# Kernel tuning notes

Measured on AMD Instinct MI355X. Metric: run time of the kernel, lower is better.

The kernel has to match this reference:

```python
import jax, jax.numpy as jnp
import numpy as np

D_MODEL = 768
MIMO_RANK = 4


def setup_inputs() -> dict:
    key = jax.random.key(0)
    ks = jax.random.split(key, 6)
    B, T, D, R = 2, 2048, D_MODEL, MIMO_RANK
    x = jax.random.normal(ks[0], (B, T, D), dtype=jnp.float32)
    norm_w = jnp.ones((D,), dtype=jnp.float32)
    W_in = jax.random.normal(ks[1], (D * R * 2, D), dtype=jnp.float32) * 0.02
    W_out = jax.random.normal(ks[2], (D, D), dtype=jnp.float32) * 0.02
    a_param = jax.random.normal(ks[3], (D, R, 2), dtype=jnp.float32) * 0.12
    b_param = jax.random.normal(ks[4], (D, R, 2), dtype=jnp.float32) * 0.15
    c_param = jax.random.normal(ks[5], (D, R, 2), dtype=jnp.float32) * 0.15
    return {"x": x, "norm_w": norm_w, "W_in": W_in, "W_out": W_out,
            "a_param": a_param, "b_param": b_param, "c_param": c_param}


def reference(x, norm_w, W_in, W_out, a_param, b_param, c_param):
    B, T, D = x.shape
    R = a_param.shape[1]
    # RMSNorm
    xn = x * jax.lax.rsqrt(jnp.mean(x * x, axis=-1, keepdims=True) + 1e-6) * norm_w
    # in_proj -> interleaved complex MIMO input u: [B,T,D,R,2]
    u = (xn @ W_in.T).reshape(B, T, D, R, 2)
    # coefficients (tanh-bounded; |a| scaled by 0.97 for stability)
    a = jnp.tanh(a_param) * 0.97
    b = jnp.tanh(b_param)
    c = jnp.tanh(c_param)
    ac = jax.lax.complex(a[..., 0], a[..., 1])  # [D,R]
    bc = jax.lax.complex(b[..., 0], b[..., 1])
    cc = jax.lax.complex(c[..., 0], c[..., 1])
    uc = jax.lax.complex(u[..., 0], u[..., 1])  # [B,T,D,R]
    # linear complex recurrence s_t = a * s_{t-1} + b * u_t, zero init state,
    # parallelized with an associative scan over time.
    bu = bc[None, None] * uc
    A = jnp.broadcast_to(ac[None, None], bu.shape)

    def comb(l, r):
        return (l[0] * r[0], r[0] * l[1] + r[1])

    _, s = jax.lax.associative_scan(comb, (A, bu), axis=1)  # [B,T,D,R] complex
    # output mix: real part of c * h, summed over MIMO rank -> [B,T,D]
    y = jnp.real(cc[None, None] * s).sum(axis=-1)
    return y @ W_out.T
```

## Files before the change

kernel.cpp:

```cpp
#include <hip/hip_runtime.h>
#include <hip/hip_bf16.h>
#include <stdint.h>

#define BATCH 2
#define TT 2048
#define DM 768
#define RR 4
#define M_TOK 4096
#define NFEAT 6144
#define NCH 6144
#define CHUNK 64
#define NCHUNK 32

typedef __attribute__((ext_vector_type(8))) short short8;
typedef __attribute__((ext_vector_type(4))) float float4v;

__device__ inline float bf2f(uint32_t bits16) {
    union { uint32_t u; float f; } x; x.u = bits16 << 16; return x.f;
}

typedef const __attribute__((address_space(1))) void* gptr_t;
typedef __attribute__((address_space(3))) void* lptr_t;

__device__ inline void async_ld16(const void* g, void* l) {
    __builtin_amdgcn_global_load_lds((gptr_t)(uintptr_t)g, (lptr_t)(uintptr_t)l,
                                     16, 0, 0);
}

__device__ inline void store_c(__hip_bfloat16* C, size_t idx, float v) {
    C[idx] = __float2bfloat16(v);
}
__device__ inline void store_c(float* C, size_t idx, float v) { C[idx] = v; }

__device__ inline uint2 pack4bf(float a, float b, float c, float d) {
    union { __hip_bfloat16 h[4]; uint2 u; } o;
    o.h[0] = __float2bfloat16(a); o.h[1] = __float2bfloat16(b);
    o.h[2] = __float2bfloat16(c); o.h[3] = __float2bfloat16(d);
    return o.u;
}

__device__ inline float2 cmul(float2 a, float2 b) {
    return make_float2(a.x * b.x - a.y * b.y, a.x * b.y + a.y * b.x);
}
__device__ inline float2 cmad(float2 a, float2 b, float2 c) {
    return make_float2(a.x * b.x - a.y * b.y + c.x,
                       a.x * b.y + a.y * b.x + c.y);
}
__device__ inline float2 csq(float2 a) {
    return make_float2(a.x * a.x - a.y * a.y, 2.f * a.x * a.y);
}

__device__ inline void cstep(float& sr, float& si, float2 a, float2 bb,
                             uint32_t uw) {
    float ur = bf2f(uw & 0xffffu), ui = bf2f(uw >> 16);
    float tr = bb.x * ur - bb.y * ui;
    float ti = bb.x * ui + bb.y * ur;
    float nr = a.x * sr - a.y * si + tr;
    float ni = a.x * si + a.y * sr + ti;
    sr = nr; si = ni;
}

__global__ __launch_bounds__(256) void prep_rms(
    const float* __restrict__ x, const float* __restrict__ w,
    const float* __restrict__ W_in, const float* __restrict__ W_out,
    const float* __restrict__ ap, const float* __restrict__ bp,
    const float* __restrict__ cp,
    __hip_bfloat16* __restrict__ xn,
    __hip_bfloat16* __restrict__ Win_bf, __hip_bfloat16* __restrict__ Wout_bf,
    float2* __restrict__ ac, float2* __restrict__ bc,
    float2* __restrict__ cc, float2* __restrict__ aQ,
    float2* __restrict__ aL) {
    int bid = blockIdx.x;
    int tid = threadIdx.x;
    if (bid < M_TOK) {
        __shared__ float wsum[3];
        float4 v = make_float4(0.f, 0.f, 0.f, 0.f);
        if (tid < 192) v = ((const float4*)(x + (size_t)bid * DM))[tid];
        float ss = v.x * v.x + v.y * v.y + v.z * v.z + v.w * v.w;
        #pragma unroll
        for (int o = 1; o < 64; o <<= 1) ss += __shfl_xor(ss, o);
        if (tid < 192 && (tid & 63) == 0) wsum[tid >> 6] = ss;
        __syncthreads();
        if (tid < 192) {
            float tot = wsum[0] + wsum[1] + wsum[2];
            float scale = rsqrtf(tot * (1.f / DM) + 1e-6f);
            float4 wv = ((const float4*)w)[tid];
            ((uint2*)(xn + (size_t)bid * DM))[tid] =
                pack4bf(v.x * scale * wv.x, v.y * scale * wv.y,
                        v.z * scale * wv.z, v.w * scale * wv.w);
        }
        return;
    }
    const int N1 = NFEAT * DM / 4;
    const int N2 = DM * DM / 4;
    int i = (bid - M_TOK) * 256 + tid;
    if (i < N1) {
        float4 v = ((const float4*)W_in)[i];
        ((uint2*)Win_bf)[i] = pack4bf(v.x, v.y, v.z, v.w);
    } else if (i < N1 + N2) {
        int k = i - N1;
        float4 v = ((const float4*)W_out)[k];
        ((uint2*)Wout_bf)[k] = pack4bf(v.x, v.y, v.z, v.w);
    }
    if (i < DM * RR) {
        float ar = tanhf(ap[2 * i])     * 0.97f;
        float ai = tanhf(ap[2 * i + 1]) * 0.97f;
        ac[i] = make_float2(ar, ai);
        bc[i] = make_float2(tanhf(bp[2 * i]), tanhf(bp[2 * i + 1]));
        cc[i] = make_float2(tanhf(cp[2 * i]), tanhf(cp[2 * i + 1]));
        float xr = ar, xi = ai;
        #pragma unroll
        for (int k = 0; k < 4; ++k) {
            float nr = xr * xr - xi * xi;
            float ni = 2.f * xr * xi;
            xr = nr; xi = ni;
        }
        aQ[i] = make_float2(xr, xi);
        #pragma unroll
        for (int k = 0; k < 2; ++k) {
            float nr = xr * xr - xi * xi;
            float ni = 2.f * xr * xi;
            xr = nr; xi = ni;
        }
        aL[i] = make_float2(xr, xi);
    }
}

template <int BM, int BN, int BK, typename OutT>
__device__ inline void gemm_body(
    const __hip_bfloat16* __restrict__ A, const __hip_bfloat16* __restrict__ B,
    OutT* __restrict__ C, int K, int ldc) {
    constexpr int MI = BM / 32;
    constexpr int NJ = BN / 32;
    constexpr int CPR = BK / 8;
    __shared__ __attribute__((aligned(16))) __hip_bfloat16 lA[BM * BK];
    __shared__ __attribute__((aligned(16))) __hip_bfloat16 lB[BN * BK];
    const int tid  = threadIdx.x;
    const int lane = tid & 63;
    const int wave = tid >> 6;
    const int quad = lane >> 4;
    const int l15  = lane & 15;
    const int wm = (wave >> 1) * (BM / 2);
    const int wn = (wave & 1) * (BN / 2);
    const int m0 = blockIdx.y * BM;
    const int n0 = blockIdx.x * BN;

    float4v acc[MI][NJ] = {};

    for (int k0 = 0; k0 < K; k0 += BK) {
        __syncthreads();
        #pragma unroll
        for (int it = 0; it < BM * CPR / 256; ++it) {
            int p = it * 256 + tid;
            int row = p / CPR;
            int cg = (p & (CPR - 1)) ^ (row & (CPR - 1));
            async_ld16(A + (size_t)(m0 + row) * K + k0 + cg * 8, lA + p * 8);
        }
        #pragma unroll
        for (int it = 0; it < BN * CPR / 256; ++it) {
            int p = it * 256 + tid;
            int row = p / CPR;
            int cg = (p & (CPR - 1)) ^ (row & (CPR - 1));
            async_ld16(B + (size_t)(n0 + row) * K + k0 + cg * 8, lB + p * 8);
        }
        __syncthreads();
        #pragma unroll
        for (int s = 0; s < BK / 32; ++s) {
            short8 af[MI], bfr[NJ];
            #pragma unroll
            for (int i = 0; i < MI; ++i) {
                int r = wm + i * 16 + l15;
                int c = (s * 4 + quad) ^ (r & (CPR - 1));
                af[i] = *(const short8*)(lA + r * BK + c * 8);
            }
            #pragma unroll
            for (int j = 0; j < NJ; ++j) {
                int r = wn + j * 16 + l15;
                int c = (s * 4 + quad) ^ (r & (CPR - 1));
                bfr[j] = *(const short8*)(lB + r * BK + c * 8);
            }
            #pragma unroll
            for (int i = 0; i < MI; ++i)
                #pragma unroll
                for (int j = 0; j < NJ; ++j)
                    acc[i][j] = __builtin_amdgcn_mfma_f32_16x16x32_bf16(
                        af[i], bfr[j], acc[i][j], 0, 0, 0);
        }
    }
    #pragma unroll
    for (int i = 0; i < MI; ++i)
        #pragma unroll
        for (int j = 0; j < NJ; ++j)
            #pragma unroll
            for (int rg = 0; rg < 4; ++rg) {
                int row = m0 + wm + i * 16 + quad * 4 + rg;
                int col = n0 + wn + j * 16 + l15;
                store_c(C, (size_t)row * ldc + col, acc[i][j][rg]);
            }
}

__global__ __launch_bounds__(256) void gemm_in(
    const __hip_bfloat16* __restrict__ A, const __hip_bfloat16* __restrict__ B,
    __hip_bfloat16* __restrict__ C, int K) {
    gemm_body<128, 128, 64, __hip_bfloat16>(A, B, C, K, NFEAT);
}

__global__ __launch_bounds__(256) void gemm_out(
    const __hip_bfloat16* __restrict__ A, const __hip_bfloat16* __restrict__ B,
    float* __restrict__ C, int K) {
    gemm_body<64, 64, 128, float>(A, B, C, K, DM);
}

__global__ __launch_bounds__(256) void scan_local2(
    const uint4* __restrict__ u4,
    const float2* __restrict__ ac, const float2* __restrict__ bc,
    const float2* __restrict__ cc,
    __hip_bfloat16* __restrict__ y_local,
    float2* __restrict__ chunkEnd) {
    __shared__ float2 se[1024];
    const int tid   = threadIdx.x;
    const int d_loc = tid & 31;
    const int s8    = tid >> 5;
    const int bd    = blockIdx.x;
    const int b     = bd >= 24;
    const int dg    = bd - b * 24;
    const int d_g   = dg * 32 + d_loc;
    const int cb    = d_g * RR;
    const int j     = blockIdx.y;

    float2 a0 = ac[cb], a1 = ac[cb + 1], a2 = ac[cb + 2], a3 = ac[cb + 3];
    float2 b0 = bc[cb], b1 = bc[cb + 1], b2 = bc[cb + 2], b3 = bc[cb + 3];
    float2 c0 = cc[cb], c1 = cc[cb + 1], c2 = cc[cb + 2], c3 = cc[cb + 3];

    const int token0 = b * TT + j * CHUNK + s8 * 8;
    const size_t base = (size_t)token0 * DM + d_g;

    uint4 uw[8];
    #pragma unroll
    for (int i = 0; i < 8; ++i) uw[i] = u4[base + (size_t)i * DM];
    float s0r = 0, s0i = 0, s1r = 0, s1i = 0;
    float s2r = 0, s2i = 0, s3r = 0, s3i = 0;
    float yloc[8];
    #pragma unroll
    for (int i = 0; i < 8; ++i) {
        cstep(s0r, s0i, a0, b0, uw[i].x);
        cstep(s1r, s1i, a1, b1, uw[i].y);
        cstep(s2r, s2i, a2, b2, uw[i].z);
        cstep(s3r, s3i, a3, b3, uw[i].w);
        yloc[i] = c0.x * s0r - c0.y * s0i + c1.x * s1r - c1.y * s1i
                + c2.x * s2r - c2.y * s2i + c3.x * s3r - c3.y * s3i;
    }
    se[tid * 4]     = make_float2(s0r, s0i);
    se[tid * 4 + 1] = make_float2(s1r, s1i);
    se[tid * 4 + 2] = make_float2(s2r, s2i);
    se[tid * 4 + 3] = make_float2(s3r, s3i);
    __syncthreads();

    float2 aE0 = csq(csq(csq(a0))), aE1 = csq(csq(csq(a1)));
    float2 aE2 = csq(csq(csq(a2))), aE3 = csq(csq(csq(a3)));
    float2 C0 = make_float2(0, 0), C1 = C0, C2 = C0, C3 = C0;
    for (int k = 0; k < s8; ++k) {
        int kb = (k * 32 + d_loc) * 4;
        C0 = cmad(C0, aE0, se[kb]);
        C1 = cmad(C1, aE1, se[kb + 1]);
        C2 = cmad(C2, aE2, se[kb + 2]);
        C3 = cmad(C3, aE3, se[kb + 3]);
    }
    if (s8 == 7) {
        size_t eb = (size_t)j * NCH + b * (DM * RR) + cb;
        chunkEnd[eb]     = cmad(C0, aE0, make_float2(s0r, s0i));
        chunkEnd[eb + 1] = cmad(C1, aE1, make_float2(s1r, s1i));
        chunkEnd[eb + 2] = cmad(C2, aE2, make_float2(s2r, s2i));
        chunkEnd[eb + 3] = cmad(C3, aE3, make_float2(s3r, s3i));
    }
    float2 q0 = cmul(cmul(c0, C0), a0);
    float2 q1 = cmul(cmul(c1, C1), a1);
    float2 q2 = cmul(cmul(c2, C2), a2);
    float2 q3 = cmul(cmul(c3, C3), a3);
    #pragma unroll
    for (int i = 0; i < 8; ++i) {
        float yv = yloc[i] + q0.x + q1.x + q2.x + q3.x;
        y_local[base + (size_t)i * DM] = __float2bfloat16(yv);
        q0 = cmul(q0, a0); q1 = cmul(q1, a1);
        q2 = cmul(q2, a2); q3 = cmul(q3, a3);
    }
}

__global__ __launch_bounds__(256) void scan_fix(
    const __hip_bfloat16* __restrict__ y_local,
    const float2* __restrict__ ac, const float2* __restrict__ cc,
    const float2* __restrict__ aQp, const float2* __restrict__ aLp,
    const float2* __restrict__ chunkEnd,
    __hip_bfloat16* __restrict__ y) {
    int g = blockIdx.x * 256 + threadIdx.x;
    int j = blockIdx.y;
    int z = blockIdx.z;
    int b = g >= DM;
    int d = g - b * DM;
    int cb = d * RR;
    float2 a0 = ac[cb], a1 = ac[cb + 1], a2 = ac[cb + 2], a3 = ac[cb + 3];
    float2 aL0 = aLp[cb], aL1 = aLp[cb + 1], aL2 = aLp[cb + 2], aL3 = aLp[cb + 3];
    float2 k0 = make_float2(0, 0), k1 = k0, k2 = k0, k3 = k0;
    for (int jj = 0; jj < j; ++jj) {
        size_t eb = (size_t)jj * NCH + b * (DM * RR) + cb;
        float2 e0 = chunkEnd[eb],     e1 = chunkEnd[eb + 1];
        float2 e2 = chunkEnd[eb + 2], e3 = chunkEnd[eb + 3];
        k0 = cmad(k0, aL0, e0); k1 = cmad(k1, aL1, e1);
        k2 = cmad(k2, aL2, e2); k3 = cmad(k3, aL3, e3);
    }
    float2 q0 = cmul(cmul(cc[cb],     k0), a0);
    float2 q1 = cmul(cmul(cc[cb + 1], k1), a1);
    float2 q2 = cmul(cmul(cc[cb + 2], k2), a2);
    float2 q3 = cmul(cmul(cc[cb + 3], k3), a3);
    float2 aQ0 = aQp[cb], aQ1 = aQp[cb + 1], aQ2 = aQp[cb + 2], aQ3 = aQp[cb + 3];
    for (int zz = 0; zz < z; ++zz) {
        q0 = cmul(q0, aQ0); q1 = cmul(q1, aQ1);
        q2 = cmul(q2, aQ2); q3 = cmul(q3, aQ3);
    }
    size_t base = ((size_t)(b * TT + j * CHUNK + z * 16)) * DM + d;
    #pragma unroll 4
    for (int i = 0; i < 16; ++i) {
        float yv = bf2f(((const uint16_t*)y_local)[base + (size_t)i * DM])
                 + q0.x + q1.x + q2.x + q3.x;
        y[base + (size_t)i * DM] = __float2bfloat16(yv);
        q0 = cmul(q0, a0); q1 = cmul(q1, a1);
        q2 = cmul(q2, a2); q3 = cmul(q3, a3);
    }
}

extern "C" void kernel_launch(void* const* d_in, const int* in_sizes, int n_in,
                              void* d_out, int out_size, void* d_ws,
                              size_t ws_size, hipStream_t stream) {
    const float* x      = (const float*)d_in[0];
    const float* norm_w = (const float*)d_in[1];
    const float* W_in   = (const float*)d_in[2];
    const float* W_out  = (const float*)d_in[3];
    const float* a_p    = (const float*)d_in[4];
    const float* b_p    = (const float*)d_in[5];
    const float* c_p    = (const float*)d_in[6];
    float* out = (float*)d_out;

    char* ws = (char*)d_ws;
    size_t off = 0;
    auto alloc = [&](size_t bytes) {
        void* p = ws + off;
        off += (bytes + 255) & ~(size_t)255;
        return p;
    };
    __hip_bfloat16* Win_bf  = (__hip_bfloat16*)alloc((size_t)NFEAT * DM * 2);
    __hip_bfloat16* Wout_bf = (__hip_bfloat16*)alloc((size_t)DM * DM * 2);
    __hip_bfloat16* xn      = (__hip_bfloat16*)alloc((size_t)M_TOK * DM * 2);
    __hip_bfloat16* u       = (__hip_bfloat16*)alloc((size_t)M_TOK * NFEAT * 2);
    __hip_bfloat16* y_local = (__hip_bfloat16*)alloc((size_t)M_TOK * DM * 2);
    __hip_bfloat16* y       = (__hip_bfloat16*)alloc((size_t)M_TOK * DM * 2);
    float2* ac = (float2*)alloc((size_t)DM * RR * 8);
    float2* bc = (float2*)alloc((size_t)DM * RR * 8);
    float2* cc = (float2*)alloc((size_t)DM * RR * 8);
    float2* aQ = (float2*)alloc((size_t)DM * RR * 8);
    float2* aL = (float2*)alloc((size_t)DM * RR * 8);
    float2* chunkEnd = (float2*)alloc((size_t)NCHUNK * NCH * 8);

    {
        int cast_blocks = ((NFEAT * DM + DM * DM) / 4 + 255) / 256;
        prep_rms<<<M_TOK + cast_blocks, 256, 0, stream>>>(
            x, norm_w, W_in, W_out, a_p, b_p, c_p,
            xn, Win_bf, Wout_bf, ac, bc, cc, aQ, aL);
    }
    gemm_in<<<dim3(NFEAT / 128, M_TOK / 128), 256, 0, stream>>>(
        xn, Win_bf, u, DM);
    scan_local2<<<dim3(48, NCHUNK), 256, 0, stream>>>(
        (const uint4*)u, ac, bc, cc, y_local, chunkEnd);
    scan_fix<<<dim3(BATCH * DM / 256, NCHUNK, 4), 256, 0, stream>>>(
        y_local, ac, cc, aQ, aL, chunkEnd, y);
    gemm_out<<<dim3(DM / 64, M_TOK / 64), 256, 0, stream>>>(
        y, Wout_bf, out, DM);
}
```

Measured before the change: 175.8 us.

## Add sequential carry-scan kernel and simplify scan_fix to use precomputed carries

Adds a carry_scan kernel that walks the chunk-end states once per channel and writes the exclusive prefix carry into chunkEnd in place. Previously every scan_fix block recomputed the prefix over all earlier chunks, which is quadratic in chunk count. scan_fix now reads that carry directly, uses a different thread layout (32 d per block, 8 tokens per thread group), and updates y_local in place instead of writing a separate y buffer. This costs one extra small sequential kernel launch with 32 dependent steps per thread.

```diff
diff --git a/kernel.cpp b/kernel.cpp
--- a/kernel.cpp
+++ b/kernel.cpp
@@ -68,8 +68,7 @@
     __hip_bfloat16* __restrict__ xn,
     __hip_bfloat16* __restrict__ Win_bf, __hip_bfloat16* __restrict__ Wout_bf,
     float2* __restrict__ ac, float2* __restrict__ bc,
-    float2* __restrict__ cc, float2* __restrict__ aQ,
-    float2* __restrict__ aL) {
+    float2* __restrict__ cc, float2* __restrict__ aL) {
     int bid = blockIdx.x;
     int tid = threadIdx.x;
     if (bid < M_TOK) {
@@ -110,14 +109,7 @@
         cc[i] = make_float2(tanhf(cp[2 * i]), tanhf(cp[2 * i + 1]));
         float xr = ar, xi = ai;
         #pragma unroll
-        for (int k = 0; k < 4; ++k) {
-            float nr = xr * xr - xi * xi;
-            float ni = 2.f * xr * xi;
-            xr = nr; xi = ni;
-        }
-        aQ[i] = make_float2(xr, xi);
-        #pragma unroll
-        for (int k = 0; k < 2; ++k) {
+        for (int k = 0; k < 6; ++k) {
             float nr = xr * xr - xi * xi;
             float ni = 2.f * xr * xi;
             xr = nr; xi = ni;
@@ -286,43 +278,59 @@
     }
 }
 
+__global__ __launch_bounds__(256) void carry_scan(
+    float2* __restrict__ chunkEnd,
+    const float2* __restrict__ aLp) {
+    int ch = blockIdx.x * 256 + threadIdx.x;
+    int dr = (ch >= DM * RR) ? ch - DM * RR : ch;
+    float2 aL = aLp[dr];
+    float2 K = make_float2(0.f, 0.f);
+    for (int j = 0; j < NCHUNK; ++j) {
+        size_t idx = (size_t)j * NCH + ch;
+        float2 e = chunkEnd[idx];
+        chunkEnd[idx] = K;
+        K = cmad(K, aL, e);
+    }
+}
+
 __global__ __launch_bounds__(256) void scan_fix(
-    const __hip_bfloat16* __restrict__ y_local,
+    __hip_bfloat16* __restrict__ y_local,
     const float2* __restrict__ ac, const float2* __restrict__ cc,
-    const float2* __restrict__ aQp, const float2* __restrict__ aLp,
-    const float2* __restrict__ chunkEnd,
-    __hip_bfloat16* __restrict__ y) {
-    int g = blockIdx.x * 256 + threadIdx.x;
-    int j = blockIdx.y;
-    int z = blockIdx.z;
-    int b = g >= DM;
-    int d = g - b * DM;
-    int cb = d * RR;
+    const float2* __restrict__ carry) {
+    const int tid   = threadIdx.x;
+    const int d_loc = tid & 31;
+    const int s8    = tid >> 5;
+    const int bd    = blockIdx.x;
+    const int b     = bd >= 24;
+    const int dg    = bd - b * 24;
+    const int d_g   = dg * 32 + d_loc;
+    const int cb    = d_g * RR;
+    const int j     = blockIdx.y;
+    const size_t kb = (size_t)j * NCH + b * (DM * RR) + cb;
+
     float2 a0 = ac[cb], a1 = ac[cb + 1], a2 = ac[cb + 2], a3 = ac[cb + 3];
-    float2 aL0 = aLp[cb], aL1 = aLp[cb + 1], aL2 = aLp[cb + 2], aL3 = aLp[cb + 3];
-    float2 k0 = make_float2(0, 0), k1 = k0, k2 = k0, k3 = k0;
-    for (int jj = 0; jj < j; ++jj) {
-        size_t eb = (size_t)jj * NCH + b * (DM * RR) + cb;
-        float2 e0 = chunkEnd[eb],     e1 = chunkEnd[eb + 1];
-        float2 e2 = chunkEnd[eb + 2], e3 = chunkEnd[eb + 3];
-        k0 = cmad(k0, aL0, e0); k1 = cmad(k1, aL1, e1);
-        k2 = cmad(k2, aL2, e2); k3 = cmad(k3, aL3, e3);
-    }
-    float2 q0 = cmul(cmul(cc[cb],     k0), a0);
-    float2 q1 = cmul(cmul(cc[cb + 1], k1), a1);
-    float2 q2 = cmul(cmul(cc[cb + 2], k2), a2);
-    float2 q3 = cmul(cmul(cc[cb + 3], k3), a3);
-    float2 aQ0 = aQp[cb], aQ1 = aQp[cb + 1], aQ2 = aQp[cb + 2], aQ3 = aQp[cb + 3];
-    for (int zz = 0; zz < z; ++zz) {
-        q0 = cmul(q0, aQ0); q1 = cmul(q1, aQ1);
-        q2 = cmul(q2, aQ2); q3 = cmul(q3, aQ3);
-    }
-    size_t base = ((size_t)(b * TT + j * CHUNK + z * 16)) * DM + d;
-    #pragma unroll 4
-    for (int i = 0; i < 16; ++i) {
-        float yv = bf2f(((const uint16_t*)y_local)[base + (size_t)i * DM])
+    float2 c0 = cc[cb], c1 = cc[cb + 1], c2 = cc[cb + 2], c3 = cc[cb + 3];
+    float2 K0 = carry[kb],     K1 = carry[kb + 1];
+    float2 K2 = carry[kb + 2], K3 = carry[kb + 3];
+
+    float2 aE0 = csq(csq(csq(a0))), aE1 = csq(csq(csq(a1)));
+    float2 aE2 = csq(csq(csq(a2))), aE3 = csq(csq(csq(a3)));
+    float2 q0 = cmul(cmul(c0, K0), a0);
+    float2 q1 = cmul(cmul(c1, K1), a1);
+    float2 q2 = cmul(cmul(c2, K2), a2);
+    float2 q3 = cmul(cmul(c3, K3), a3);
+    for (int t = 0; t < s8; ++t) {
+        q0 = cmul(q0, aE0); q1 = cmul(q1, aE1);
+        q2 = cmul(q2, aE2); q3 = cmul(q3, aE3);
+    }
+    const int token0 = b * TT + j * CHUNK + s8 * 8;
+    const size_t base = (size_t)token0 * DM + d_g;
+    #pragma unroll
+    for (int i = 0; i < 8; ++i) {
+        size_t idx = base + (size_t)i * DM;
+        float yv = bf2f(((const uint16_t*)y_local)[idx])
                  + q0.x + q1.x + q2.x + q3.x;
-        y[base + (size_t)i * DM] = __float2bfloat16(yv);
+        y_local[idx] = __float2bfloat16(yv);
         q0 = cmul(q0, a0); q1 = cmul(q1, a1);
         q2 = cmul(q2, a2); q3 = cmul(q3, a3);
     }
@@ -352,11 +360,9 @@
     __hip_bfloat16* xn      = (__hip_bfloat16*)alloc((size_t)M_TOK * DM * 2);
     __hip_bfloat16* u       = (__hip_bfloat16*)alloc((size_t)M_TOK * NFEAT * 2);
     __hip_bfloat16* y_local = (__hip_bfloat16*)alloc((size_t)M_TOK * DM * 2);
-    __hip_bfloat16* y       = (__hip_bfloat16*)alloc((size_t)M_TOK * DM * 2);
     float2* ac = (float2*)alloc((size_t)DM * RR * 8);
     float2* bc = (float2*)alloc((size_t)DM * RR * 8);
     float2* cc = (float2*)alloc((size_t)DM * RR * 8);
-    float2* aQ = (float2*)alloc((size_t)DM * RR * 8);
     float2* aL = (float2*)alloc((size_t)DM * RR * 8);
     float2* chunkEnd = (float2*)alloc((size_t)NCHUNK * NCH * 8);
 
@@ -364,14 +370,15 @@
         int cast_blocks = ((NFEAT * DM + DM * DM) / 4 + 255) / 256;
         prep_rms<<<M_TOK + cast_blocks, 256, 0, stream>>>(
             x, norm_w, W_in, W_out, a_p, b_p, c_p,
-            xn, Win_bf, Wout_bf, ac, bc, cc, aQ, aL);
+            xn, Win_bf, Wout_bf, ac, bc, cc, aL);
     }
     gemm_in<<<dim3(NFEAT / 128, M_TOK / 128), 256, 0, stream>>>(
         xn, Win_bf, u, DM);
     scan_local2<<<dim3(48, NCHUNK), 256, 0, stream>>>(
         (const uint4*)u, ac, bc, cc, y_local, chunkEnd);
-    scan_fix<<<dim3(BATCH * DM / 256, NCHUNK, 4), 256, 0, stream>>>(
-        y_local, ac, cc, aQ, aL, chunkEnd, y);
+    carry_scan<<<NCH / 256, 256, 0, stream>>>(chunkEnd, aL);
+    scan_fix<<<dim3(48, NCHUNK), 256, 0, stream>>>(
+        y_local, ac, cc, chunkEnd);
     gemm_out<<<dim3(DM / 64, M_TOK / 64), 256, 0, stream>>>(
-        y, Wout_bf, out, DM);
-}
+        y_local, Wout_bf, out, DM);
+}
```

Result: faster. 172.1 us (-2.1%).
